# Kernel tuning notes

Measured on AMD Instinct MI355X. Metric: run time of the kernel, lower is better.

Reference implementation:

```python
import jax, jax.numpy as jnp
import numpy as np
from jax import lax

B, T, I, H, L, O = 256, 512, 64, 256, 2, 1


def _lstm_dir(x, w_ih, w_hh, b_ih, b_hh, reverse):
    # x: [B,T,Din]; w_ih: [4H,Din]; w_hh: [4H,H]; biases: [4H]
    Bn = x.shape[0]
    Hn = w_hh.shape[1]
    # precompute input projection for all timesteps
    xp = jnp.einsum('btd,gd->btg', x, w_ih) + b_ih + b_hh  # [B,T,4H]
    xp = jnp.swapaxes(xp, 0, 1)  # [T,B,4H]
    h0 = jnp.zeros((Bn, Hn), x.dtype)
    c0 = jnp.zeros((Bn, Hn), x.dtype)

    def step(carry, g_t):
        h, c = carry
        gates = g_t + h @ w_hh.T  # [B,4H]
        i, f, g, o = jnp.split(gates, 4, axis=-1)  # PyTorch gate order
        c = jax.nn.sigmoid(f) * c + jax.nn.sigmoid(i) * jnp.tanh(g)
        h = jax.nn.sigmoid(o) * jnp.tanh(c)
        return (h, c), h

    _, hs = lax.scan(step, (h0, c0), xp, reverse=reverse)  # hs: [T,B,H], time-aligned
    return jnp.swapaxes(hs, 0, 1)  # [B,T,H]


def setup_inputs() -> dict:
    key = jax.random.key(0)
    ks = jax.random.split(key, 20)
    s = 1.0 / np.sqrt(H)
    u = lambda k, shp: jax.random.uniform(k, shp, jnp.float32, -s, s)
    d = {
        'x': jax.random.normal(ks[0], (B, T, I), jnp.float32),
        # layer 0, forward and reverse directions
        'w_ih_l0': u(ks[1], (4 * H, I)), 'w_hh_l0': u(ks[2], (4 * H, H)),
        'b_ih_l0': u(ks[3], (4 * H,)), 'b_hh_l0': u(ks[4], (4 * H,)),
        'w_ih_l0r': u(ks[5], (4 * H, I)), 'w_hh_l0r': u(ks[6], (4 * H, H)),
        'b_ih_l0r': u(ks[7], (4 * H,)), 'b_hh_l0r': u(ks[8], (4 * H,)),
        # layer 1 (input dim = 2H from bidirectional concat)
        'w_ih_l1': u(ks[9], (4 * H, 2 * H)), 'w_hh_l1': u(ks[10], (4 * H, H)),
        'b_ih_l1': u(ks[11], (4 * H,)), 'b_hh_l1': u(ks[12], (4 * H,)),
        'w_ih_l1r': u(ks[13], (4 * H, 2 * H)), 'w_hh_l1r': u(ks[14], (4 * H, H)),
        'b_ih_l1r': u(ks[15], (4 * H,)), 'b_hh_l1r': u(ks[16], (4 * H,)),
        # fc head
        'fc_w': u(ks[17], (O, 2 * H)), 'fc_b': u(ks[18], (O,)),
    }
    return d


def reference(x, w_ih_l0, w_hh_l0, b_ih_l0, b_hh_l0,
              w_ih_l0r, w_hh_l0r, b_ih_l0r, b_hh_l0r,
              w_ih_l1, w_hh_l1, b_ih_l1, b_hh_l1,
              w_ih_l1r, w_hh_l1r, b_ih_l1r, b_hh_l1r,
              fc_w, fc_b):
    # layer 0
    h_fwd = _lstm_dir(x, w_ih_l0, w_hh_l0, b_ih_l0, b_hh_l0, reverse=False)
    h_bwd = _lstm_dir(x, w_ih_l0r, w_hh_l0r, b_ih_l0r, b_hh_l0r, reverse=True)
    h = jnp.concatenate([h_fwd, h_bwd], axis=-1)  # [B,T,2H]
    # layer 1
    h_fwd = _lstm_dir(h, w_ih_l1, w_hh_l1, b_ih_l1, b_hh_l1, reverse=False)
    h_bwd = _lstm_dir(h, w_ih_l1r, w_hh_l1r, b_ih_l1r, b_hh_l1r, reverse=True)
    h = jnp.concatenate([h_fwd, h_bwd], axis=-1)  # [B,T,2H]
    # fc on last timestep
    return h[:, -1, :] @ fc_w.T + fc_b  # [B,O]
```

## Files before the change

### kernel.cpp

```cpp
#include <hip/hip_runtime.h>

typedef __bf16 bf16_t;
typedef bf16_t bf16x8 __attribute__((ext_vector_type(8)));
typedef bf16_t bf16x4 __attribute__((ext_vector_type(4)));
typedef float f32x4 __attribute__((ext_vector_type(4)));

#define B_SZ 256
#define T_SZ 512
#define H_SZ 256
#define SCOPE_AGENT __HIP_MEMORY_SCOPE_AGENT
#define SENT32 0x7FC17FC1u

__device__ __forceinline__ float sigm(float x) { return 1.f / (1.f + __expf(-x)); }
__device__ __forceinline__ float tanhx(float x) {
  x = fminf(fmaxf(x, -15.f), 15.f);
  float e = __expf(-2.f * x);
  return (1.f - e) / (1.f + e);
}
__device__ __forceinline__ uint32_t pack_bf16x2(float a, float b) {
  union { bf16_t h[2]; uint32_t u; } v;
  v.h[0] = (bf16_t)a; v.h[1] = (bf16_t)b; return v.u;
}
__device__ __forceinline__ void st32_agent(uint32_t* p, uint32_t v) {
  __hip_atomic_store(p, v, __ATOMIC_RELAXED, SCOPE_AGENT);
}
__device__ __forceinline__ uint64_t ld64_agent(const uint64_t* p) {
  return __hip_atomic_load(p, __ATOMIC_RELAXED, SCOPE_AGENT);
}
__device__ __forceinline__ bool okv(uint64_t v) {
  return ((uint32_t)v != SENT32) & ((uint32_t)(v >> 32) != SENT32);
}
#define MFMA(a, b, c) __builtin_amdgcn_mfma_f32_16x16x32_bf16((a), (b), (c), 0, 0, 0)

__global__ __launch_bounds__(512, 2) void l0_scan(
    const bf16_t* __restrict__ xbf,
    const bf16_t* __restrict__ wih_f, const bf16_t* __restrict__ whhhi_f,
    const bf16_t* __restrict__ whhlo_f, const float* __restrict__ bias_f,
    const bf16_t* __restrict__ wih_b, const bf16_t* __restrict__ whhhi_b,
    const bf16_t* __restrict__ whhlo_b, const float* __restrict__ bias_b,
    bf16_t* __restrict__ h0) {
  const int id = blockIdx.x;
  const int ct = id >> 5;
  const int g  = id & 31;
  const int dir = g >> 4, bt = g & 15;
  const bf16_t* __restrict__ wih  = dir ? wih_b : wih_f;
  const bf16_t* __restrict__ whhh = dir ? whhhi_b : whhhi_f;
  const bf16_t* __restrict__ whhl = dir ? whhlo_b : whhlo_f;
  const float*  __restrict__ bias = dir ? bias_b : bias_f;

  const int tid = threadIdx.x;
  const int lane = tid & 63, wv = tid >> 6, l15 = lane & 15, quad = lane >> 4;
  const int b0 = bt * 16;

  __shared__ bf16_t hbl[16][264];
  __shared__ float  gl[16][132];

  const int gc = wv * 16 + l15;
  const int row = (gc >> 5) * H_SZ + ct * 32 + (gc & 31);
  bf16x8 wfi[2], wfh[8], wfl[8];
#pragma unroll
  for (int kt = 0; kt < 2; ++kt)
    wfi[kt] = *(const bf16x8*)(wih + (size_t)row * 64 + kt * 32 + quad * 8);
#pragma unroll
  for (int kt = 0; kt < 8; ++kt) {
    wfh[kt] = *(const bf16x8*)(whhh + (size_t)row * H_SZ + kt * 32 + quad * 8);
    wfl[kt] = *(const bf16x8*)(whhl + (size_t)row * H_SZ + kt * 32 + quad * 8);
  }
  const int et = tid & 255;
  const int erow = et >> 4, ecol = 2 * (et & 15);
  const int gj = ct * 32 + ecol;
  float bia[4][2];
#pragma unroll
  for (int gg = 0; gg < 4; ++gg) {
    bia[gg][0] = bias[gg * H_SZ + gj];
    bia[gg][1] = bias[gg * H_SZ + gj + 1];
  }
  float2 c2 = {0.f, 0.f};
  const bf16_t* xrow = xbf + (size_t)(b0 + l15) * T_SZ * 64;
  const int prow = tid >> 5, pcq = (tid & 31) * 2;

  for (int s = 0; s < T_SZ; ++s) {
    const int t = dir ? (T_SZ - 1 - s) : s;
    f32x4 acc = {0.f, 0.f, 0.f, 0.f};
#pragma unroll
    for (int kt = 0; kt < 2; ++kt) {
      bf16x8 xa = *(const bf16x8*)(xrow + t * 64 + kt * 32 + quad * 8);
      acc = MFMA(xa, wfi[kt], acc);
    }
    if (s == 0) {
      for (int i = tid; i < 16 * 264 / 2; i += 512) ((uint32_t*)hbl)[i] = 0u;
    } else {
      const int tp = dir ? (t + 1) : (t - 1);
      const uint64_t* src =
          (const uint64_t*)(h0 + ((size_t)tp * B_SZ + b0 + prow) * 512 + dir * H_SZ) + pcq;
      uint64_t v0, v1;
      for (;;) {
        v0 = ld64_agent(src); v1 = ld64_agent(src + 1);
        if (okv(v0) && okv(v1)) break;
      }
      uint64_t* dst = (uint64_t*)&hbl[prow][pcq * 4];
      dst[0] = v0; dst[1] = v1;
    }
    __syncthreads();
#pragma unroll
    for (int kt = 0; kt < 8; ++kt) {
      bf16x8 ha = *(const bf16x8*)&hbl[l15][kt * 32 + quad * 8];
      acc = MFMA(ha, wfh[kt], acc);
      acc = MFMA(ha, wfl[kt], acc);
    }
#pragma unroll
    for (int r = 0; r < 4; ++r) gl[quad * 4 + r][wv * 16 + l15] = acc[r];
    __syncthreads();
    if (tid < 256) {
      float hv[2];
#pragma unroll
      for (int u = 0; u < 2; ++u) {
        float iv = sigm(gl[erow][0 * 32 + ecol + u] + bia[0][u]);
        float fv = sigm(gl[erow][1 * 32 + ecol + u] + bia[1][u]);
        float gv = tanhx(gl[erow][2 * 32 + ecol + u] + bia[2][u]);
        float ov = sigm(gl[erow][3 * 32 + ecol + u] + bia[3][u]);
        float cp = u ? c2.y : c2.x;
        float cn = fv * cp + iv * gv;
        if (u) c2.y = cn; else c2.x = cn;
        hv[u] = ov * tanhx(cn);
      }
      st32_agent((uint32_t*)(h0 + ((size_t)t * B_SZ + b0 + erow) * 512 + dir * H_SZ + gj),
                 pack_bf16x2(hv[0], hv[1]));
    }
  }
}

__global__ __launch_bounds__(512, 2) void l1_scan(
    const bf16_t* __restrict__ h0,
    const bf16_t* __restrict__ wih, const bf16_t* __restrict__ whhh,
    const bf16_t* __restrict__ whhl, const float* __restrict__ bias,
    bf16_t* __restrict__ h1f, bf16_t* __restrict__ hg1) {
  const int id = blockIdx.x;
  const int ct = id >> 4, bt = id & 15;
  bf16_t* hgs = hg1 + (size_t)bt * T_SZ * 4096;

  const int tid = threadIdx.x;
  const int lane = tid & 63, wv = tid >> 6, l15 = lane & 15, quad = lane >> 4;
  const int b0 = bt * 16;

  __shared__ bf16_t ibl[2][16][520];
  __shared__ bf16_t hbl[16][264];
  __shared__ float  gl[16][132];

  const int gc = wv * 16 + l15;
  const int row = (gc >> 5) * H_SZ + ct * 32 + (gc & 31);
  bf16x8 wfi[16], wfh[8], wfl[8];
#pragma unroll
  for (int kt = 0; kt < 16; ++kt)
    wfi[kt] = *(const bf16x8*)(wih + (size_t)row * 512 + kt * 32 + quad * 8);
#pragma unroll
  for (int kt = 0; kt < 8; ++kt) {
    wfh[kt] = *(const bf16x8*)(whhh + (size_t)row * H_SZ + kt * 32 + quad * 8);
    wfl[kt] = *(const bf16x8*)(whhl + (size_t)row * H_SZ + kt * 32 + quad * 8);
  }
  const int et = tid & 255;
  const int erow = et >> 4, ecol = 2 * (et & 15);
  const int gj = ct * 32 + ecol;
  float bia[4][2];
#pragma unroll
  for (int g = 0; g < 4; ++g) {
    bia[g][0] = bias[g * H_SZ + gj];
    bia[g][1] = bias[g * H_SZ + gj + 1];
  }
  float2 c2 = {0.f, 0.f};
  const int prow = tid >> 5, pcq = (tid & 31) * 2;
  const int fr = tid >> 5, fcc = (tid & 31) * 16;

  {
    const bf16_t* src = h0 + ((size_t)(b0 + fr)) * 512 + fcc;
    *(bf16x8*)&ibl[0][fr][fcc]     = *(const bf16x8*)(src);
    *(bf16x8*)&ibl[0][fr][fcc + 8] = *(const bf16x8*)(src + 8);
  }
  __syncthreads();

  for (int s = 0; s < T_SZ; ++s) {
    const int cur = s & 1, nxt = cur ^ 1;
    bf16x8 pf0, pf1;
    if (s + 1 < T_SZ) {
      const bf16_t* src = h0 + ((size_t)(s + 1) * B_SZ + b0 + fr) * 512 + fcc;
      pf0 = *(const bf16x8*)(src);
      pf1 = *(const bf16x8*)(src + 8);
    }
    f32x4 acc = {0.f, 0.f, 0.f, 0.f};
#pragma unroll
    for (int kt = 0; kt < 16; ++kt) {
      bf16x8 a = *(const bf16x8*)&ibl[cur][l15][kt * 32 + quad * 8];
      acc = MFMA(a, wfi[kt], acc);
    }
    if (s == 0) {
      for (int i = tid; i < 16 * 264 / 2; i += 512) ((uint32_t*)hbl)[i] = 0u;
    } else {
      const uint64_t* src =
          (const uint64_t*)(hgs + (size_t)(s - 1) * 4096 + prow * H_SZ) + pcq;
      uint64_t v0, v1;
      for (;;) {
        v0 = ld64_agent(src); v1 = ld64_agent(src + 1);
        if (okv(v0) && okv(v1)) break;
      }
      uint64_t* dst = (uint64_t*)&hbl[prow][pcq * 4];
      dst[0] = v0; dst[1] = v1;
    }
    if (s + 1 < T_SZ) {
      *(bf16x8*)&ibl[nxt][fr][fcc]     = pf0;
      *(bf16x8*)&ibl[nxt][fr][fcc + 8] = pf1;
    }
    __syncthreads();
#pragma unroll
    for (int kt = 0; kt < 8; ++kt) {
      bf16x8 ha = *(const bf16x8*)&hbl[l15][kt * 32 + quad * 8];
      acc = MFMA(ha, wfh[kt], acc);
      acc = MFMA(ha, wfl[kt], acc);
    }
#pragma unroll
    for (int r = 0; r < 4; ++r) gl[quad * 4 + r][wv * 16 + l15] = acc[r];
    __syncthreads();
    if (tid < 256) {
      float hv[2];
#pragma unroll
      for (int u = 0; u < 2; ++u) {
        float iv = sigm(gl[erow][0 * 32 + ecol + u] + bia[0][u]);
        float fv = sigm(gl[erow][1 * 32 + ecol + u] + bia[1][u]);
        float gv = tanhx(gl[erow][2 * 32 + ecol + u] + bia[2][u]);
        float ov = sigm(gl[erow][3 * 32 + ecol + u] + bia[3][u]);
        float cp = u ? c2.y : c2.x;
        float cn = fv * cp + iv * gv;
        if (u) c2.y = cn; else c2.x = cn;
        hv[u] = ov * tanhx(cn);
      }
      uint32_t pk = pack_bf16x2(hv[0], hv[1]);
      st32_agent((uint32_t*)(hgs + (size_t)s * 4096 + erow * H_SZ + gj), pk);
      if (s == T_SZ - 1)
        *(uint32_t*)(h1f + (size_t)(b0 + erow) * H_SZ + gj) = pk;
    }
  }
}

__global__ __launch_bounds__(256) void l1b_step(
    const bf16_t* __restrict__ h0, const bf16_t* __restrict__ wih_r,
    const float* __restrict__ bias_r, bf16_t* __restrict__ h1b) {
  const int bt = blockIdx.x >> 2, ct = blockIdx.x & 3;
  const int tid = threadIdx.x, lane = tid & 63, wv = tid >> 6;
  const int l15 = lane & 15, quad = lane >> 4;
  const int c0 = ct * 64 + wv * 16;
  const bf16_t* arow = h0 + ((size_t)(T_SZ - 1) * B_SZ + bt * 16 + l15) * 512;
  f32x4 acc[4] = {{0,0,0,0},{0,0,0,0},{0,0,0,0},{0,0,0,0}};
#pragma unroll 4
  for (int kt = 0; kt < 16; ++kt) {
    bf16x8 a = *(const bf16x8*)(arow + kt * 32 + quad * 8);
#pragma unroll
    for (int g = 0; g < 4; ++g) {
      bf16x8 w = *(const bf16x8*)(wih_r + (size_t)(g * H_SZ + c0 + l15) * 512 + kt * 32 + quad * 8);
      acc[g] = MFMA(a, w, acc[g]);
    }
  }
  const int j = c0 + l15;
  const float bi = bias_r[j], bg = bias_r[2 * H_SZ + j], bo = bias_r[3 * H_SZ + j];
#pragma unroll
  for (int r = 0; r < 4; ++r) {
    const int row = bt * 16 + quad * 4 + r;
    float iv = sigm(acc[0][r] + bi);
    float gv = tanhx(acc[2][r] + bg);
    float ov = sigm(acc[3][r] + bo);
    float cn = iv * gv;
    h1b[(size_t)row * H_SZ + j] = (bf16_t)(ov * tanhx(cn));
  }
}

__global__ void k_cvt4(const float* __restrict__ s, bf16_t* __restrict__ d, int n4) {
  int i = blockIdx.x * 256 + threadIdx.x;
  if (i < n4) {
    float4 v = ((const float4*)s)[i];
    bf16x4 o; o[0] = (bf16_t)v.x; o[1] = (bf16_t)v.y; o[2] = (bf16_t)v.z; o[3] = (bf16_t)v.w;
    ((bf16x4*)d)[i] = o;
  }
}
__global__ void k_split(const float* __restrict__ s, bf16_t* __restrict__ hi,
                        bf16_t* __restrict__ lo, int n) {
  int i = blockIdx.x * 256 + threadIdx.x;
  if (i < n) {
    float v = s[i];
    bf16_t h = (bf16_t)v;
    hi[i] = h;
    lo[i] = (bf16_t)(v - (float)h);
  }
}
__global__ void k_bias(const float* __restrict__ a, const float* __restrict__ b,
                       float* __restrict__ d, int n) {
  int i = blockIdx.x * 256 + threadIdx.x;
  if (i < n) d[i] = a[i] + b[i];
}
__global__ void k_fill4(uint4* __restrict__ p, int n) {
  int i = blockIdx.x * 256 + threadIdx.x;
  if (i < n) p[i] = make_uint4(SENT32, SENT32, SENT32, SENT32);
}
__global__ void k_fc(const bf16_t* __restrict__ hf, const bf16_t* __restrict__ hb,
                     const float* __restrict__ fw, const float* __restrict__ fb,
                     float* __restrict__ out) {
  int b = threadIdx.x;
  float s = fb[0];
  const bf16_t* pf = hf + (size_t)b * H_SZ;
  const bf16_t* pb = hb + (size_t)b * H_SZ;
  for (int j = 0; j < H_SZ; ++j) s += fw[j] * (float)pf[j];
  for (int j = 0; j < H_SZ; ++j) s += fw[H_SZ + j] * (float)pb[j];
  out[b] = s;
}

extern "C" void kernel_launch(void* const* d_in, const int* in_sizes, int n_in,
                              void* d_out, int out_size, void* d_ws, size_t ws_size,
                              hipStream_t stream) {
  (void)in_sizes; (void)n_in; (void)out_size; (void)ws_size;
  const float* x      = (const float*)d_in[0];
  const float* wih[4] = {(const float*)d_in[1], (const float*)d_in[5],
                         (const float*)d_in[9], (const float*)d_in[13]};
  const float* whh[4] = {(const float*)d_in[2], (const float*)d_in[6],
                         (const float*)d_in[10], (const float*)d_in[14]};
  const float* bih[4] = {(const float*)d_in[3], (const float*)d_in[7],
                         (const float*)d_in[11], (const float*)d_in[15]};
  const float* bhh[4] = {(const float*)d_in[4], (const float*)d_in[8],
                         (const float*)d_in[12], (const float*)d_in[16]};
  const float* fcw = (const float*)d_in[17];
  const float* fcb = (const float*)d_in[18];
  float* out = (float*)d_out;

  char* p = (char*)d_ws;
  auto take = [&](size_t bytes) { char* r = p; p += (bytes + 255) & ~(size_t)255; return r; };
  const int KinL[4] = {64, 64, 512, 512};
  bf16_t* wihb[4]; float* biasc[4]; bf16_t* whhhi[3]; bf16_t* whhlo[3];
  for (int k = 0; k < 4; ++k) {
    wihb[k]  = (bf16_t*)take((size_t)1024 * KinL[k] * 2);
    biasc[k] = (float*)take(1024 * 4);
  }
  for (int k = 0; k < 3; ++k) {
    whhhi[k] = (bf16_t*)take((size_t)1024 * 256 * 2);
    whhlo[k] = (bf16_t*)take((size_t)1024 * 256 * 2);
  }
  bf16_t* xbf = (bf16_t*)take((size_t)B_SZ * T_SZ * 64 * 2);
  bf16_t* h1f = (bf16_t*)take((size_t)B_SZ * H_SZ * 2);
  bf16_t* h1b = (bf16_t*)take((size_t)B_SZ * H_SZ * 2);
  char* sbeg = p;
  bf16_t* h0  = (bf16_t*)take((size_t)T_SZ * B_SZ * 512 * 2);
  bf16_t* hg1 = (bf16_t*)take((size_t)16 * T_SZ * 4096 * 2);
  size_t sbytes = (size_t)(p - sbeg);

  k_cvt4<<<dim3(8192), 256, 0, stream>>>(x, xbf, (B_SZ * T_SZ * 64) / 4);
  for (int k = 0; k < 4; ++k) {
    k_cvt4<<<dim3((1024 * KinL[k] / 4 + 255) / 256), 256, 0, stream>>>(
        wih[k], wihb[k], 1024 * KinL[k] / 4);
    k_bias<<<dim3(4), 256, 0, stream>>>(bih[k], bhh[k], biasc[k], 1024);
  }
  for (int k = 0; k < 3; ++k)
    k_split<<<dim3(1024), 256, 0, stream>>>(whh[k], whhhi[k], whhlo[k], 1024 * 256);
  {
    int n4 = (int)(sbytes / 16);
    k_fill4<<<dim3((n4 + 255) / 256), 256, 0, stream>>>((uint4*)sbeg, n4);
  }

  l0_scan<<<dim3(256), 512, 0, stream>>>(
      xbf, wihb[0], whhhi[0], whhlo[0], biasc[0],
           wihb[1], whhhi[1], whhlo[1], biasc[1], h0);
  l1_scan<<<dim3(128), 512, 0, stream>>>(
      h0, wihb[2], whhhi[2], whhlo[2], biasc[2], h1f, hg1);
  l1b_step<<<dim3(64), 256, 0, stream>>>(h0, wihb[3], biasc[3], h1b);

  k_fc<<<dim3(1), 256, 0, stream>>>(h1f, h1b, fcw, fcb, out);
}
```

Measured before the change: 2.082 ms.

## Halve layer-0 scan blocks with 64-column tiles and keep own hidden slice locally

The layer-0 recurrent scan now gives each block 64 hidden columns instead of 32. Each wave holds two weight tiles and runs two MFMA accumulators, and all 512 threads do the elementwise gate work. This halves the number of cooperating blocks from 256 to 128, which means fewer cross-block flag polls per timestep. Both scans also write their own h slice straight into shared memory and skip polling global memory for it. The costs are double the register pressure for weights and more serial MFMA work per block.

```diff
diff --git a/kernel.cpp b/kernel.cpp
--- a/kernel.cpp
+++ b/kernel.cpp
@@ -53,22 +53,24 @@
   const int b0 = bt * 16;
 
   __shared__ bf16_t hbl[16][264];
-  __shared__ float  gl[16][132];
-
-  const int gc = wv * 16 + l15;
-  const int row = (gc >> 5) * H_SZ + ct * 32 + (gc & 31);
-  bf16x8 wfi[2], wfh[8], wfl[8];
-#pragma unroll
-  for (int kt = 0; kt < 2; ++kt)
-    wfi[kt] = *(const bf16x8*)(wih + (size_t)row * 64 + kt * 32 + quad * 8);
-#pragma unroll
-  for (int kt = 0; kt < 8; ++kt) {
-    wfh[kt] = *(const bf16x8*)(whhh + (size_t)row * H_SZ + kt * 32 + quad * 8);
-    wfl[kt] = *(const bf16x8*)(whhl + (size_t)row * H_SZ + kt * 32 + quad * 8);
-  }
-  const int et = tid & 255;
-  const int erow = et >> 4, ecol = 2 * (et & 15);
-  const int gj = ct * 32 + ecol;
+  __shared__ float  gl[16][260];
+
+  bf16x8 wfi[2][2], wfh[2][8], wfl[2][8];
+#pragma unroll
+  for (int p = 0; p < 2; ++p) {
+    const int gc = (wv * 2 + p) * 16 + l15;
+    const int row = (gc >> 6) * H_SZ + ct * 64 + (gc & 63);
+#pragma unroll
+    for (int kt = 0; kt < 2; ++kt)
+      wfi[p][kt] = *(const bf16x8*)(wih + (size_t)row * 64 + kt * 32 + quad * 8);
+#pragma unroll
+    for (int kt = 0; kt < 8; ++kt) {
+      wfh[p][kt] = *(const bf16x8*)(whhh + (size_t)row * H_SZ + kt * 32 + quad * 8);
+      wfl[p][kt] = *(const bf16x8*)(whhl + (size_t)row * H_SZ + kt * 32 + quad * 8);
+    }
+  }
+  const int erow = tid >> 5, ecol = 2 * (tid & 31);
+  const int gj = ct * 64 + ecol;
   float bia[4][2];
 #pragma unroll
   for (int gg = 0; gg < 4; ++gg) {
@@ -78,18 +80,20 @@
   float2 c2 = {0.f, 0.f};
   const bf16_t* xrow = xbf + (size_t)(b0 + l15) * T_SZ * 64;
   const int prow = tid >> 5, pcq = (tid & 31) * 2;
+  const bool own = ((tid & 31) >> 3) == ct;
 
   for (int s = 0; s < T_SZ; ++s) {
     const int t = dir ? (T_SZ - 1 - s) : s;
-    f32x4 acc = {0.f, 0.f, 0.f, 0.f};
+    f32x4 acc0 = {0.f, 0.f, 0.f, 0.f}, acc1 = {0.f, 0.f, 0.f, 0.f};
 #pragma unroll
     for (int kt = 0; kt < 2; ++kt) {
       bf16x8 xa = *(const bf16x8*)(xrow + t * 64 + kt * 32 + quad * 8);
-      acc = MFMA(xa, wfi[kt], acc);
+      acc0 = MFMA(xa, wfi[0][kt], acc0);
+      acc1 = MFMA(xa, wfi[1][kt], acc1);
     }
     if (s == 0) {
       for (int i = tid; i < 16 * 264 / 2; i += 512) ((uint32_t*)hbl)[i] = 0u;
-    } else {
+    } else if (!own) {
       const int tp = dir ? (t + 1) : (t - 1);
       const uint64_t* src =
           (const uint64_t*)(h0 + ((size_t)tp * B_SZ + b0 + prow) * 512 + dir * H_SZ) + pcq;
@@ -105,27 +109,34 @@
 #pragma unroll
     for (int kt = 0; kt < 8; ++kt) {
       bf16x8 ha = *(const bf16x8*)&hbl[l15][kt * 32 + quad * 8];
-      acc = MFMA(ha, wfh[kt], acc);
-      acc = MFMA(ha, wfl[kt], acc);
-    }
-#pragma unroll
-    for (int r = 0; r < 4; ++r) gl[quad * 4 + r][wv * 16 + l15] = acc[r];
+      acc0 = MFMA(ha, wfh[0][kt], acc0);
+      acc0 = MFMA(ha, wfl[0][kt], acc0);
+      acc1 = MFMA(ha, wfh[1][kt], acc1);
+      acc1 = MFMA(ha, wfl[1][kt], acc1);
+    }
+#pragma unroll
+    for (int r = 0; r < 4; ++r) {
+      gl[quad * 4 + r][(wv * 2 + 0) * 16 + l15] = acc0[r];
+      gl[quad * 4 + r][(wv * 2 + 1) * 16 + l15] = acc1[r];
+    }
     __syncthreads();
-    if (tid < 256) {
+    {
       float hv[2];
 #pragma unroll
       for (int u = 0; u < 2; ++u) {
-        float iv = sigm(gl[erow][0 * 32 + ecol + u] + bia[0][u]);
-        float fv = sigm(gl[erow][1 * 32 + ecol + u] + bia[1][u]);
-        float gv = tanhx(gl[erow][2 * 32 + ecol + u] + bia[2][u]);
-        float ov = sigm(gl[erow][3 * 32 + ecol + u] + bia[3][u]);
+        float iv = sigm(gl[erow][0 * 64 + ecol + u] + bia[0][u]);
+        float fv = sigm(gl[erow][1 * 64 + ecol + u] + bia[1][u]);
+        float gv = tanhx(gl[erow][2 * 64 + ecol + u] + bia[2][u]);
+        float ov = sigm(gl[erow][3 * 64 + ecol + u] + bia[3][u]);
         float cp = u ? c2.y : c2.x;
         float cn = fv * cp + iv * gv;
         if (u) c2.y = cn; else c2.x = cn;
         hv[u] = ov * tanhx(cn);
       }
+      uint32_t pk = pack_bf16x2(hv[0], hv[1]);
       st32_agent((uint32_t*)(h0 + ((size_t)t * B_SZ + b0 + erow) * 512 + dir * H_SZ + gj),
-                 pack_bf16x2(hv[0], hv[1]));
+                 pk);
+      *(uint32_t*)&hbl[erow][gj] = pk;
     }
   }
 }
@@ -169,6 +180,7 @@
   }
   float2 c2 = {0.f, 0.f};
   const int prow = tid >> 5, pcq = (tid & 31) * 2;
+  const bool own = ((tid & 31) >> 2) == ct;
   const int fr = tid >> 5, fcc = (tid & 31) * 16;
 
   {
@@ -194,7 +206,7 @@
     }
     if (s == 0) {
       for (int i = tid; i < 16 * 264 / 2; i += 512) ((uint32_t*)hbl)[i] = 0u;
-    } else {
+    } else if (!own) {
       const uint64_t* src =
           (const uint64_t*)(hgs + (size_t)(s - 1) * 4096 + prow * H_SZ) + pcq;
       uint64_t v0, v1;
@@ -234,6 +246,7 @@
       }
       uint32_t pk = pack_bf16x2(hv[0], hv[1]);
       st32_agent((uint32_t*)(hgs + (size_t)s * 4096 + erow * H_SZ + gj), pk);
+      *(uint32_t*)&hbl[erow][gj] = pk;
       if (s == T_SZ - 1)
         *(uint32_t*)(h1f + (size_t)(b0 + erow) * H_SZ + gj) = pk;
     }
@@ -360,7 +373,7 @@
     k_fill4<<<dim3((n4 + 255) / 256), 256, 0, stream>>>((uint4*)sbeg, n4);
   }
 
-  l0_scan<<<dim3(256), 512, 0, stream>>>(
+  l0_scan<<<dim3(128), 512, 0, stream>>>(
       xbf, wihb[0], whhhi[0], whhlo[0], biasc[0],
            wihb[1], whhhi[1], whhlo[1], biasc[1], h0);
   l1_scan<<<dim3(128), 512, 0, stream>>>(
```

New measurement: 2.110 ms. About the same (+1.3%).

## Remap block ids, widen gate epilogue to 4 columns, and back off polling

Applied to the files above, without the earlier changes.

Changes the l0 block index mapping so the 8 column tiles of one batch/direction group get consecutive block ids, which likely places them close together for cross-block communication. The gate epilogue now runs on 128 threads that each handle 4 hidden units and publish them with a single 64-bit agent-scope store instead of 32-bit stores, so fewer stores go through the cross-block handoff. The spin-wait loops now call s_sleep between polls to reduce memory traffic from polling. The cost is more serial transcendental work per thread on the critical path, plus possible extra wakeup latency from the sleep.

```diff
diff --git a/kernel.cpp b/kernel.cpp
--- a/kernel.cpp
+++ b/kernel.cpp
@@ -17,11 +17,7 @@
   float e = __expf(-2.f * x);
   return (1.f - e) / (1.f + e);
 }
-__device__ __forceinline__ uint32_t pack_bf16x2(float a, float b) {
-  union { bf16_t h[2]; uint32_t u; } v;
-  v.h[0] = (bf16_t)a; v.h[1] = (bf16_t)b; return v.u;
-}
-__device__ __forceinline__ void st32_agent(uint32_t* p, uint32_t v) {
+__device__ __forceinline__ void st64_agent(uint64_t* p, uint64_t v) {
   __hip_atomic_store(p, v, __ATOMIC_RELAXED, SCOPE_AGENT);
 }
 __device__ __forceinline__ uint64_t ld64_agent(const uint64_t* p) {
@@ -40,9 +36,7 @@
     const bf16_t* __restrict__ whhlo_b, const float* __restrict__ bias_b,
     bf16_t* __restrict__ h0) {
   const int id = blockIdx.x;
-  const int ct = id >> 5;
-  const int g  = id & 31;
-  const int dir = g >> 4, bt = g & 15;
+  const int dir = id >> 7, bt = (id >> 3) & 15, ct = id & 7;
   const bf16_t* __restrict__ wih  = dir ? wih_b : wih_f;
   const bf16_t* __restrict__ whhh = dir ? whhhi_b : whhhi_f;
   const bf16_t* __restrict__ whhl = dir ? whhlo_b : whhlo_f;
@@ -66,16 +60,16 @@
     wfh[kt] = *(const bf16x8*)(whhh + (size_t)row * H_SZ + kt * 32 + quad * 8);
     wfl[kt] = *(const bf16x8*)(whhl + (size_t)row * H_SZ + kt * 32 + quad * 8);
   }
-  const int et = tid & 255;
-  const int erow = et >> 4, ecol = 2 * (et & 15);
-  const int gj = ct * 32 + ecol;
-  float bia[4][2];
-#pragma unroll
-  for (int gg = 0; gg < 4; ++gg) {
-    bia[gg][0] = bias[gg * H_SZ + gj];
-    bia[gg][1] = bias[gg * H_SZ + gj + 1];
-  }
-  float2 c2 = {0.f, 0.f};
+  const int erow = tid >> 3, ecg = (tid & 7) * 4;
+  const int gj = ct * 32 + ecg;
+  float bia[4][4];
+  if (tid < 128) {
+#pragma unroll
+    for (int gg = 0; gg < 4; ++gg)
+#pragma unroll
+      for (int k = 0; k < 4; ++k) bia[gg][k] = bias[gg * H_SZ + gj + k];
+  }
+  float c4[4] = {0.f, 0.f, 0.f, 0.f};
   const bf16_t* xrow = xbf + (size_t)(b0 + l15) * T_SZ * 64;
   const int prow = tid >> 5, pcq = (tid & 31) * 2;
 
@@ -93,10 +87,10 @@
       const int tp = dir ? (t + 1) : (t - 1);
       const uint64_t* src =
           (const uint64_t*)(h0 + ((size_t)tp * B_SZ + b0 + prow) * 512 + dir * H_SZ) + pcq;
-      uint64_t v0, v1;
-      for (;;) {
+      uint64_t v0 = ld64_agent(src), v1 = ld64_agent(src + 1);
+      while (!(okv(v0) && okv(v1))) {
+        __builtin_amdgcn_s_sleep(1);
         v0 = ld64_agent(src); v1 = ld64_agent(src + 1);
-        if (okv(v0) && okv(v1)) break;
       }
       uint64_t* dst = (uint64_t*)&hbl[prow][pcq * 4];
       dst[0] = v0; dst[1] = v1;
@@ -111,21 +105,20 @@
 #pragma unroll
     for (int r = 0; r < 4; ++r) gl[quad * 4 + r][wv * 16 + l15] = acc[r];
     __syncthreads();
-    if (tid < 256) {
-      float hv[2];
-#pragma unroll
-      for (int u = 0; u < 2; ++u) {
-        float iv = sigm(gl[erow][0 * 32 + ecol + u] + bia[0][u]);
-        float fv = sigm(gl[erow][1 * 32 + ecol + u] + bia[1][u]);
-        float gv = tanhx(gl[erow][2 * 32 + ecol + u] + bia[2][u]);
-        float ov = sigm(gl[erow][3 * 32 + ecol + u] + bia[3][u]);
-        float cp = u ? c2.y : c2.x;
-        float cn = fv * cp + iv * gv;
-        if (u) c2.y = cn; else c2.x = cn;
-        hv[u] = ov * tanhx(cn);
+    if (tid < 128) {
+      union { bf16_t h[4]; uint64_t u; } pk;
+#pragma unroll
+      for (int k = 0; k < 4; ++k) {
+        float iv = sigm(gl[erow][0 * 32 + ecg + k] + bia[0][k]);
+        float fv = sigm(gl[erow][1 * 32 + ecg + k] + bia[1][k]);
+        float gv = tanhx(gl[erow][2 * 32 + ecg + k] + bia[2][k]);
+        float ov = sigm(gl[erow][3 * 32 + ecg + k] + bia[3][k]);
+        float cn = fv * c4[k] + iv * gv;
+        c4[k] = cn;
+        pk.h[k] = (bf16_t)(ov * tanhx(cn));
       }
-      st32_agent((uint32_t*)(h0 + ((size_t)t * B_SZ + b0 + erow) * 512 + dir * H_SZ + gj),
-                 pack_bf16x2(hv[0], hv[1]));
+      st64_agent((uint64_t*)(h0 + ((size_t)t * B_SZ + b0 + erow) * 512 + dir * H_SZ + gj),
+                 pk.u);
     }
   }
 }
@@ -158,16 +151,16 @@
     wfh[kt] = *(const bf16x8*)(whhh + (size_t)row * H_SZ + kt * 32 + quad * 8);
     wfl[kt] = *(const bf16x8*)(whhl + (size_t)row * H_SZ + kt * 32 + quad * 8);
   }
-  const int et = tid & 255;
-  const int erow = et >> 4, ecol = 2 * (et & 15);
-  const int gj = ct * 32 + ecol;
-  float bia[4][2];
-#pragma unroll
-  for (int g = 0; g < 4; ++g) {
-    bia[g][0] = bias[g * H_SZ + gj];
-    bia[g][1] = bias[g * H_SZ + gj + 1];
-  }
-  float2 c2 = {0.f, 0.f};
+  const int erow = tid >> 3, ecg = (tid & 7) * 4;
+  const int gj = ct * 32 + ecg;
+  float bia[4][4];
+  if (tid < 128) {
+#pragma unroll
+    for (int g = 0; g < 4; ++g)
+#pragma unroll
+      for (int k = 0; k < 4; ++k) bia[g][k] = bias[g * H_SZ + gj + k];
+  }
+  float c4[4] = {0.f, 0.f, 0.f, 0.f};
   const int prow = tid >> 5, pcq = (tid & 31) * 2;
   const int fr = tid >> 5, fcc = (tid & 31) * 16;
 
@@ -197,10 +190,10 @@
     } else {
       const uint64_t* src =
           (const uint64_t*)(hgs + (size_t)(s - 1) * 4096 + prow * H_SZ) + pcq;
-      uint64_t v0, v1;
-      for (;;) {
+      uint64_t v0 = ld64_agent(src), v1 = ld64_agent(src + 1);
+      while (!(okv(v0) && okv(v1))) {
+        __builtin_amdgcn_s_sleep(1);
         v0 = ld64_agent(src); v1 = ld64_agent(src + 1);
-        if (okv(v0) && okv(v1)) break;
       }
       uint64_t* dst = (uint64_t*)&hbl[prow][pcq * 4];
       dst[0] = v0; dst[1] = v1;
@@ -219,23 +212,21 @@
 #pragma unroll
     for (int r = 0; r < 4; ++r) gl[quad * 4 + r][wv * 16 + l15] = acc[r];
     __syncthreads();
-    if (tid < 256) {
-      float hv[2];
-#pragma unroll
-      for (int u = 0; u < 2; ++u) {
-        float iv = sigm(gl[erow][0 * 32 + ecol + u] + bia[0][u]);
-        float fv = sigm(gl[erow][1 * 32 + ecol + u] + bia[1][u]);
-        float gv = tanhx(gl[erow][2 * 32 + ecol + u] + bia[2][u]);
-        float ov = sigm(gl[erow][3 * 32 + ecol + u] + bia[3][u]);
-        float cp = u ? c2.y : c2.x;
-        float cn = fv * cp + iv * gv;
-        if (u) c2.y = cn; else c2.x = cn;
-        hv[u] = ov * tanhx(cn);
+    if (tid < 128) {
+      union { bf16_t h[4]; uint64_t u; } pk;
+#pragma unroll
+      for (int k = 0; k < 4; ++k) {
+        float iv = sigm(gl[erow][0 * 32 + ecg + k] + bia[0][k]);
+        float fv = sigm(gl[erow][1 * 32 + ecg + k] + bia[1][k]);
+        float gv = tanhx(gl[erow][2 * 32 + ecg + k] + bia[2][k]);
+        float ov = sigm(gl[erow][3 * 32 + ecg + k] + bia[3][k]);
+        float cn = fv * c4[k] + iv * gv;
+        c4[k] = cn;
+        pk.h[k] = (bf16_t)(ov * tanhx(cn));
       }
-      uint32_t pk = pack_bf16x2(hv[0], hv[1]);
-      st32_agent((uint32_t*)(hgs + (size_t)s * 4096 + erow * H_SZ + gj), pk);
+      st64_agent((uint64_t*)(hgs + (size_t)s * 4096 + erow * H_SZ + gj), pk.u);
       if (s == T_SZ - 1)
-        *(uint32_t*)(h1f + (size_t)(b0 + erow) * H_SZ + gj) = pk;
+        *(uint64_t*)(h1f + (size_t)(b0 + erow) * H_SZ + gj) = pk.u;
     }
   }
 }
```

New measurement: 2.901 ms. 39.3% more time.
